# Performance work log

Measured on AMD Instinct MI355X. Metric: run time of the kernel, lower is better.

The kernel has to match this reference:

```python
import jax, jax.numpy as jnp
import numpy as np

B, T, IN, H, OUT = 4096, 256, 2, 50, 2


def _rnn_layer(x, W_ih, W_hh, b_ih, b_hh):
    # x: [B, T, F] -> out: [B, T, H]. Elman RNN: h_t = tanh(W_ih x_t + b_ih + W_hh h_{t-1} + b_hh)
    pre = jnp.einsum('btf,hf->bth', x, W_ih) + b_ih + b_hh  # input projection hoisted out of scan
    h0 = jnp.zeros((x.shape[0], W_hh.shape[0]), dtype=x.dtype)

    def step(h, pre_t):
        h = jnp.tanh(pre_t + h @ W_hh.T)
        return h, h

    _, hs = jax.lax.scan(step, h0, jnp.swapaxes(pre, 0, 1))  # scan over time: [T, B, H]
    return jnp.swapaxes(hs, 0, 1)


def setup_inputs() -> dict:
    key = jax.random.key(0)
    ks = jax.random.split(key, 16)
    s_in = 1.0 / np.sqrt(H)  # torch nn.RNN init: U(-1/sqrt(H), 1/sqrt(H))

    def u(k, shape):
        return jax.random.uniform(k, shape, jnp.float32, -s_in, s_in)

    return {
        'x': jax.random.normal(ks[0], (B, T, IN), jnp.float32),
        'W_ih1': u(ks[1], (H, IN)), 'W_hh1': u(ks[2], (H, H)), 'b_ih1': u(ks[3], (H,)), 'b_hh1': u(ks[4], (H,)),
        'W_ih2': u(ks[5], (H, H)), 'W_hh2': u(ks[6], (H, H)), 'b_ih2': u(ks[7], (H,)), 'b_hh2': u(ks[8], (H,)),
        'W_ih3': u(ks[9], (H, H)), 'W_hh3': u(ks[10], (H, H)), 'b_ih3': u(ks[11], (H,)), 'b_hh3': u(ks[12], (H,)),
        'fc_w': u(ks[13], (OUT, H)), 'fc_b': u(ks[14], (OUT,)),
    }


def reference(x, W_ih1, W_hh1, b_ih1, b_hh1, W_ih2, W_hh2, b_ih2, b_hh2,
              W_ih3, W_hh3, b_ih3, b_hh3, fc_w, fc_b):
    out = _rnn_layer(x, W_ih1, W_hh1, b_ih1, b_hh1)
    out = _rnn_layer(out, W_ih2, W_hh2, b_ih2, b_hh2)
    out = _rnn_layer(out, W_ih3, W_hh3, b_ih3, b_hh3)
    return out[:, -1, :] @ fc_w.T + fc_b  # [B, OUT]
```

## Files before the change

### kernel.cpp

```cpp
#include <hip/hip_runtime.h>
#include <hip/hip_fp16.h>

namespace {

constexpr int T_STEPS = 256;
constexpr int HD = 50;
constexpr int HP = 64;
constexpr int KST = 88;
constexpr int KSTS = 72;
constexpr int BT = 16;
constexpr int NTHR = 768;
constexpr int XST = 34;
constexpr int LAY_SH = BT * KST;
constexpr int SLOT_SH = 3 * LAY_SH;

typedef __attribute__((ext_vector_type(8))) _Float16 f16x8;
typedef __attribute__((ext_vector_type(4))) float f32x4;

__device__ __forceinline__ unsigned short f2h(float x) {
  __half h = __float2half(x);
  return *reinterpret_cast<unsigned short*>(&h);
}
__device__ __forceinline__ float h2f(unsigned short u) {
  __half h;
  *reinterpret_cast<unsigned short*>(&h) = u;
  return __half2float(h);
}
__device__ __forceinline__ float fast_tanh(float x) {
  float e = __expf(2.0f * x);
  return 1.0f - 2.0f * __builtin_amdgcn_rcpf(e + 1.0f);
}

#define MFMA16 __builtin_amdgcn_mfma_f32_16x16x32_f16

__global__ __launch_bounds__(NTHR, 3) void rnn3_kernel(
    const float* __restrict__ x,
    const float* __restrict__ Wih1, const float* __restrict__ Whh1,
    const float* __restrict__ bih1, const float* __restrict__ bhh1,
    const float* __restrict__ Wih2, const float* __restrict__ Whh2,
    const float* __restrict__ bih2, const float* __restrict__ bhh2,
    const float* __restrict__ Wih3, const float* __restrict__ Whh3,
    const float* __restrict__ bih3, const float* __restrict__ bhh3,
    const float* __restrict__ fcw, const float* __restrict__ fcb,
    float* __restrict__ out) {
  __shared__ unsigned short hbuf[3 * SLOT_SH];
  __shared__ float xls[T_STEPS][XST];
  __shared__ unsigned short scr[2][HP * KSTS];

  const int tid = threadIdx.x;
  const int w = tid >> 6;
  const int myL = w >> 2;
  const int wv = w & 3;
  const int lane = tid & 63;
  const int quad = lane >> 4;
  const int l15 = lane & 15;
  const int b0 = blockIdx.x * BT;

  {
    unsigned int* hz = reinterpret_cast<unsigned int*>(hbuf);
    const int n = 3 * SLOT_SH / 2;
    for (int i = tid; i < n; i += NTHR) hz[i] = 0u;
  }
  for (int idx = tid; idx < BT * T_STEPS; idx += NTHR) {
    int b = idx >> 8, t = idx & 255;
    float2 v = *reinterpret_cast<const float2*>(x + (size_t)(b0 + b) * (T_STEPS * 2) + 2 * t);
    xls[t][2 * b] = v.x;
    xls[t][2 * b + 1] = v.y;
  }

  const float* mats[5] = {Whh1, Wih2, Whh2, Wih3, Whh3};
  constexpr int matL[5] = {0, 1, 1, 2, 2};
  constexpr int matS[5] = {0, 0, 1, 0, 1};
  f16x8 wAh[2][2], wAl[2][2];
#pragma unroll
  for (int sl = 0; sl < 2; ++sl)
#pragma unroll
    for (int ks = 0; ks < 2; ++ks) { wAh[sl][ks] = f16x8(0); wAl[sl][ks] = f16x8(0); }

  const int arow = 16 * wv + l15;
#pragma unroll
  for (int m = 0; m < 5; ++m) {
    __syncthreads();
    const float* W = mats[m];
    for (int idx = tid; idx < HP * HP; idx += NTHR) {
      int i = idx >> 6, k = idx & 63;
      float v = (i < HD && k < HD) ? W[i * HD + k] : 0.0f;
      unsigned short hi = f2h(v);
      scr[0][i * KSTS + k] = hi;
      scr[1][i * KSTS + k] = f2h((v - h2f(hi)) * 2048.0f);
    }
    __syncthreads();
    if (myL == matL[m]) {
      const int sl = matS[m];
      const unsigned short* ph = &scr[0][arow * KSTS + 8 * quad];
      const unsigned short* pl = &scr[1][arow * KSTS + 8 * quad];
      wAh[sl][0] = *reinterpret_cast<const f16x8*>(ph);
      wAh[sl][1] = *reinterpret_cast<const f16x8*>(ph + 32);
      wAl[sl][0] = *reinterpret_cast<const f16x8*>(pl);
      wAl[sl][1] = *reinterpret_cast<const f16x8*>(pl + 32);
    }
  }

  const int ic = 16 * wv + 4 * quad;
  const float* bi = (myL == 0) ? bih1 : (myL == 1) ? bih2 : bih3;
  const float* bh = (myL == 0) ? bhh1 : (myL == 1) ? bhh2 : bhh3;
  float wx0[4], wx1[4], bs[4];
#pragma unroll
  for (int r = 0; r < 4; ++r) {
    int i = ic + r;
    bool v = i < HD;
    bs[r] = v ? (bi[i] + bh[i]) : 0.0f;
    wx0[r] = (v && myL == 0) ? Wih1[i * 2 + 0] : 0.0f;
    wx1[r] = (v && myL == 0) ? Wih1[i * 2 + 1] : 0.0f;
  }

  const int selfBuf = myL;
  const int crossBuf = (myL > 0) ? myL - 1 : 0;
  const int ldsOff = l15 * KST + 8 * quad;
  constexpr float INV = 4.8828125e-4f;

  const unsigned short* sbase = hbuf + selfBuf * LAY_SH + ldsOff;
  const unsigned short* cbase = hbuf + crossBuf * LAY_SH + ldsOff;
  unsigned short* wbase = hbuf + myL * LAY_SH + l15 * KST + ic;

  f16x8 pfC0 = f16x8(0), pfC1 = f16x8(0);

  __syncthreads();

  auto step = [&](int s, int wr, int rd, bool act) {
    f16x8 bS0, bS1, pfN0, pfN1;
    if (act) {
      bS0 = *reinterpret_cast<const f16x8*>(sbase + rd * SLOT_SH);
      bS1 = *reinterpret_cast<const f16x8*>(sbase + rd * SLOT_SH + 32);
    }
    if (myL > 0) {
      pfN0 = *reinterpret_cast<const f16x8*>(cbase + rd * SLOT_SH);
      pfN1 = *reinterpret_cast<const f16x8*>(cbase + rd * SLOT_SH + 32);
    }
    if (act) {
      f32x4 c1, c2;
      if (myL == 0) {
        float2 xc = *reinterpret_cast<const float2*>(&xls[s][2 * l15]);
#pragma unroll
        for (int r = 0; r < 4; ++r) {
          c1[r] = bs[r] + wx0[r] * xc.x + wx1[r] * xc.y;
          c2[r] = 0.0f;
        }
        c1 = MFMA16(wAh[0][0], bS0, c1, 0, 0, 0);
        c2 = MFMA16(wAl[0][0], bS0, c2, 0, 0, 0);
        c1 = MFMA16(wAh[0][1], bS1, c1, 0, 0, 0);
        c2 = MFMA16(wAl[0][1], bS1, c2, 0, 0, 0);
      } else {
#pragma unroll
        for (int r = 0; r < 4; ++r) { c1[r] = bs[r]; c2[r] = 0.0f; }
        c1 = MFMA16(wAh[0][0], pfC0, c1, 0, 0, 0);
        c2 = MFMA16(wAl[0][0], pfC0, c2, 0, 0, 0);
        c1 = MFMA16(wAh[0][1], pfC1, c1, 0, 0, 0);
        c2 = MFMA16(wAl[0][1], pfC1, c2, 0, 0, 0);
        c1 = MFMA16(wAh[1][0], bS0, c1, 0, 0, 0);
        c2 = MFMA16(wAl[1][0], bS0, c2, 0, 0, 0);
        c1 = MFMA16(wAh[1][1], bS1, c1, 0, 0, 0);
        c2 = MFMA16(wAl[1][1], bS1, c2, 0, 0, 0);
      }
      unsigned short ht[4];
#pragma unroll
      for (int r = 0; r < 4; ++r) ht[r] = f2h(fast_tanh(c1[r] + c2[r] * INV));
      unsigned int h01 = (unsigned int)ht[0] | ((unsigned int)ht[1] << 16);
      unsigned int h23 = (unsigned int)ht[2] | ((unsigned int)ht[3] << 16);
      *reinterpret_cast<uint2*>(wbase + wr * SLOT_SH) = make_uint2(h01, h23);
    }
    if (myL > 0) { pfC0 = pfN0; pfC1 = pfN1; }
    __syncthreads();
  };

  auto actOf = [&](int s) {
    return (myL == 0) ? (s < T_STEPS)
         : (myL == 1) ? (s >= 2 && s < T_STEPS + 2)
                      : (s >= 4);
  };

  for (int s = 0; s < 4; ++s) step(s, s % 3, (s + 2) % 3, actOf(s));
  int sb = 4;
  for (int it = 0; it < 84; ++it, sb += 3) {
    step(sb + 0, 1, 0, true);
    step(sb + 1, 2, 1, true);
    step(sb + 2, 0, 2, true);
  }
  for (int s = 256; s < 260; ++s) step(s, s % 3, (s + 2) % 3, actOf(s));

  if (tid < BT * 2) {
    int b = tid >> 1, o = tid & 1;
    const unsigned short* h3 = hbuf + 1 * SLOT_SH + 2 * LAY_SH + b * KST;
    float acc = fcb[o];
    for (int i = 0; i < HD; ++i) acc += fcw[o * HD + i] * h2f(h3[i]);
    out[(size_t)(b0 + b) * 2 + o] = acc;
  }
}

}

extern "C" void kernel_launch(void* const* d_in, const int* in_sizes, int n_in,
                              void* d_out, int out_size, void* d_ws, size_t ws_size,
                              hipStream_t stream) {
  const float* x = (const float*)d_in[0];
  const float* Wih1 = (const float*)d_in[1];
  const float* Whh1 = (const float*)d_in[2];
  const float* bih1 = (const float*)d_in[3];
  const float* bhh1 = (const float*)d_in[4];
  const float* Wih2 = (const float*)d_in[5];
  const float* Whh2 = (const float*)d_in[6];
  const float* bih2 = (const float*)d_in[7];
  const float* bhh2 = (const float*)d_in[8];
  const float* Wih3 = (const float*)d_in[9];
  const float* Whh3 = (const float*)d_in[10];
  const float* bih3 = (const float*)d_in[11];
  const float* bhh3 = (const float*)d_in[12];
  const float* fcw = (const float*)d_in[13];
  const float* fcb = (const float*)d_in[14];

  rnn3_kernel<<<4096 / BT, NTHR, 0, stream>>>(x, Wih1, Whh1, bih1, bhh1,
                                              Wih2, Whh2, bih2, bhh2,
                                              Wih3, Whh3, bih3, bhh3,
                                              fcw, fcb, (float*)d_out);
}
```

Measured before the change: 201.7 us.

## Give each RNN layer a single wave computing all four output tiles

The block shrinks from 12 waves (4 per layer, one 16-row tile each) to 3 waves, one per layer. Each wave now keeps all four weight row-tiles in registers and issues four times as many MFMAs per step. The wave reads its own hidden state right after writing it, and the next step's x and cross-layer input are loaded before the barrier. The aim is cheaper per-step barriers with fewer waves and fewer LDS round trips, at the cost of much higher register pressure and less parallelism per block.

```diff
diff --git a/kernel.cpp b/kernel.cpp
--- a/kernel.cpp
+++ b/kernel.cpp
@@ -9,7 +9,7 @@
 constexpr int KST = 88;
 constexpr int KSTS = 72;
 constexpr int BT = 16;
-constexpr int NTHR = 768;
+constexpr int NTHR = 192;
 constexpr int XST = 34;
 constexpr int LAY_SH = BT * KST;
 constexpr int SLOT_SH = 3 * LAY_SH;
@@ -33,7 +33,7 @@
 
 #define MFMA16 __builtin_amdgcn_mfma_f32_16x16x32_f16
 
-__global__ __launch_bounds__(NTHR, 3) void rnn3_kernel(
+__global__ __launch_bounds__(NTHR, 1) void rnn3_kernel(
     const float* __restrict__ x,
     const float* __restrict__ Wih1, const float* __restrict__ Whh1,
     const float* __restrict__ bih1, const float* __restrict__ bhh1,
@@ -48,9 +48,7 @@
   __shared__ unsigned short scr[2][HP * KSTS];
 
   const int tid = threadIdx.x;
-  const int w = tid >> 6;
-  const int myL = w >> 2;
-  const int wv = w & 3;
+  const int myL = tid >> 6;
   const int lane = tid & 63;
   const int quad = lane >> 4;
   const int l15 = lane & 15;
@@ -70,14 +68,15 @@
 
   const float* mats[5] = {Whh1, Wih2, Whh2, Wih3, Whh3};
   constexpr int matL[5] = {0, 1, 1, 2, 2};
-  constexpr int matS[5] = {0, 0, 1, 0, 1};
-  f16x8 wAh[2][2], wAl[2][2];
+  constexpr int matS[5] = {1, 0, 1, 0, 1};
+  f16x8 wAh[2][4][2], wAl[2][4][2];
 #pragma unroll
   for (int sl = 0; sl < 2; ++sl)
 #pragma unroll
-    for (int ks = 0; ks < 2; ++ks) { wAh[sl][ks] = f16x8(0); wAl[sl][ks] = f16x8(0); }
-
-  const int arow = 16 * wv + l15;
+    for (int t = 0; t < 4; ++t)
+#pragma unroll
+      for (int ks = 0; ks < 2; ++ks) { wAh[sl][t][ks] = f16x8(0); wAl[sl][t][ks] = f16x8(0); }
+
 #pragma unroll
   for (int m = 0; m < 5; ++m) {
     __syncthreads();
@@ -92,84 +91,93 @@
     __syncthreads();
     if (myL == matL[m]) {
       const int sl = matS[m];
-      const unsigned short* ph = &scr[0][arow * KSTS + 8 * quad];
-      const unsigned short* pl = &scr[1][arow * KSTS + 8 * quad];
-      wAh[sl][0] = *reinterpret_cast<const f16x8*>(ph);
-      wAh[sl][1] = *reinterpret_cast<const f16x8*>(ph + 32);
-      wAl[sl][0] = *reinterpret_cast<const f16x8*>(pl);
-      wAl[sl][1] = *reinterpret_cast<const f16x8*>(pl + 32);
-    }
-  }
-
-  const int ic = 16 * wv + 4 * quad;
+#pragma unroll
+      for (int t = 0; t < 4; ++t) {
+        const int arow = 16 * t + l15;
+#pragma unroll
+        for (int ks = 0; ks < 2; ++ks) {
+          wAh[sl][t][ks] = *reinterpret_cast<const f16x8*>(&scr[0][arow * KSTS + 32 * ks + 8 * quad]);
+          wAl[sl][t][ks] = *reinterpret_cast<const f16x8*>(&scr[1][arow * KSTS + 32 * ks + 8 * quad]);
+        }
+      }
+    }
+  }
+
   const float* bi = (myL == 0) ? bih1 : (myL == 1) ? bih2 : bih3;
   const float* bh = (myL == 0) ? bhh1 : (myL == 1) ? bhh2 : bhh3;
-  float wx0[4], wx1[4], bs[4];
-#pragma unroll
-  for (int r = 0; r < 4; ++r) {
-    int i = ic + r;
-    bool v = i < HD;
-    bs[r] = v ? (bi[i] + bh[i]) : 0.0f;
-    wx0[r] = (v && myL == 0) ? Wih1[i * 2 + 0] : 0.0f;
-    wx1[r] = (v && myL == 0) ? Wih1[i * 2 + 1] : 0.0f;
-  }
-
-  const int selfBuf = myL;
-  const int crossBuf = (myL > 0) ? myL - 1 : 0;
-  const int ldsOff = l15 * KST + 8 * quad;
+  float bsc[4][4], wx0[4][4], wx1[4][4];
+  f32x4 bsv[4];
+#pragma unroll
+  for (int t = 0; t < 4; ++t)
+#pragma unroll
+    for (int r = 0; r < 4; ++r) {
+      int i = 16 * t + 4 * quad + r;
+      bool v = i < HD;
+      bsc[t][r] = v ? (bi[i] + bh[i]) : 0.0f;
+      wx0[t][r] = (v && myL == 0) ? Wih1[i * 2 + 0] : 0.0f;
+      wx1[t][r] = (v && myL == 0) ? Wih1[i * 2 + 1] : 0.0f;
+      bsv[t][r] = bsc[t][r];
+    }
+
+  const int ldsOffR = l15 * KST + 8 * quad;
+  const unsigned short* sbase = hbuf + myL * LAY_SH + ldsOffR;
+  const unsigned short* cbase = hbuf + ((myL > 0) ? myL - 1 : 0) * LAY_SH + ldsOffR;
+  unsigned short* wbase = hbuf + myL * LAY_SH + l15 * KST + 4 * quad;
   constexpr float INV = 4.8828125e-4f;
 
-  const unsigned short* sbase = hbuf + selfBuf * LAY_SH + ldsOff;
-  const unsigned short* cbase = hbuf + crossBuf * LAY_SH + ldsOff;
-  unsigned short* wbase = hbuf + myL * LAY_SH + l15 * KST + ic;
-
-  f16x8 pfC0 = f16x8(0), pfC1 = f16x8(0);
+  f16x8 bS0 = f16x8(0), bS1 = f16x8(0);
+  f16x8 pf0 = f16x8(0), pf1 = f16x8(0);
+  f32x4 zero4 = {0.f, 0.f, 0.f, 0.f};
 
   __syncthreads();
-
-  auto step = [&](int s, int wr, int rd, bool act) {
-    f16x8 bS0, bS1, pfN0, pfN1;
+  float2 xcur = (myL == 0) ? *reinterpret_cast<const float2*>(&xls[0][2 * l15])
+                           : make_float2(0.f, 0.f);
+
+  auto step = [&](int s, int wr, int rd2, bool act) {
     if (act) {
-      bS0 = *reinterpret_cast<const f16x8*>(sbase + rd * SLOT_SH);
-      bS1 = *reinterpret_cast<const f16x8*>(sbase + rd * SLOT_SH + 32);
-    }
+      f32x4 c1[4], c2[4];
+      if (myL == 0) {
+#pragma unroll
+        for (int t = 0; t < 4; ++t) {
+          f32x4 ci;
+#pragma unroll
+          for (int r = 0; r < 4; ++r) ci[r] = bsc[t][r] + wx0[t][r] * xcur.x + wx1[t][r] * xcur.y;
+          c1[t] = MFMA16(wAh[1][t][0], bS0, ci, 0, 0, 0);
+          c2[t] = MFMA16(wAl[1][t][0], bS0, zero4, 0, 0, 0);
+          c1[t] = MFMA16(wAh[1][t][1], bS1, c1[t], 0, 0, 0);
+          c2[t] = MFMA16(wAl[1][t][1], bS1, c2[t], 0, 0, 0);
+        }
+        int sn = (s + 1 < T_STEPS) ? s + 1 : T_STEPS - 1;
+        xcur = *reinterpret_cast<const float2*>(&xls[sn][2 * l15]);
+      } else {
+#pragma unroll
+        for (int t = 0; t < 4; ++t) {
+          c1[t] = MFMA16(wAh[0][t][0], pf0, bsv[t], 0, 0, 0);
+          c2[t] = MFMA16(wAl[0][t][0], pf0, zero4, 0, 0, 0);
+          c1[t] = MFMA16(wAh[0][t][1], pf1, c1[t], 0, 0, 0);
+          c2[t] = MFMA16(wAl[0][t][1], pf1, c2[t], 0, 0, 0);
+          c1[t] = MFMA16(wAh[1][t][0], bS0, c1[t], 0, 0, 0);
+          c2[t] = MFMA16(wAl[1][t][0], bS0, c2[t], 0, 0, 0);
+          c1[t] = MFMA16(wAh[1][t][1], bS1, c1[t], 0, 0, 0);
+          c2[t] = MFMA16(wAl[1][t][1], bS1, c2[t], 0, 0, 0);
+        }
+      }
+#pragma unroll
+      for (int t = 0; t < 4; ++t) {
+        unsigned short ht[4];
+#pragma unroll
+        for (int r = 0; r < 4; ++r) ht[r] = f2h(fast_tanh(c1[t][r] + c2[t][r] * INV));
+        unsigned int h01 = (unsigned int)ht[0] | ((unsigned int)ht[1] << 16);
+        unsigned int h23 = (unsigned int)ht[2] | ((unsigned int)ht[3] << 16);
+        *reinterpret_cast<uint2*>(wbase + wr * SLOT_SH + 16 * t) = make_uint2(h01, h23);
+      }
+    }
+    bS0 = *reinterpret_cast<const f16x8*>(sbase + wr * SLOT_SH);
+    bS1 = *reinterpret_cast<const f16x8*>(sbase + wr * SLOT_SH + 32);
     if (myL > 0) {
-      pfN0 = *reinterpret_cast<const f16x8*>(cbase + rd * SLOT_SH);
-      pfN1 = *reinterpret_cast<const f16x8*>(cbase + rd * SLOT_SH + 32);
-    }
-    if (act) {
-      f32x4 c1, c2;
-      if (myL == 0) {
-        float2 xc = *reinterpret_cast<const float2*>(&xls[s][2 * l15]);
-#pragma unroll
-        for (int r = 0; r < 4; ++r) {
-          c1[r] = bs[r] + wx0[r] * xc.x + wx1[r] * xc.y;
-          c2[r] = 0.0f;
-        }
-        c1 = MFMA16(wAh[0][0], bS0, c1, 0, 0, 0);
-        c2 = MFMA16(wAl[0][0], bS0, c2, 0, 0, 0);
-        c1 = MFMA16(wAh[0][1], bS1, c1, 0, 0, 0);
-        c2 = MFMA16(wAl[0][1], bS1, c2, 0, 0, 0);
-      } else {
-#pragma unroll
-        for (int r = 0; r < 4; ++r) { c1[r] = bs[r]; c2[r] = 0.0f; }
-        c1 = MFMA16(wAh[0][0], pfC0, c1, 0, 0, 0);
-        c2 = MFMA16(wAl[0][0], pfC0, c2, 0, 0, 0);
-        c1 = MFMA16(wAh[0][1], pfC1, c1, 0, 0, 0);
-        c2 = MFMA16(wAl[0][1], pfC1, c2, 0, 0, 0);
-        c1 = MFMA16(wAh[1][0], bS0, c1, 0, 0, 0);
-        c2 = MFMA16(wAl[1][0], bS0, c2, 0, 0, 0);
-        c1 = MFMA16(wAh[1][1], bS1, c1, 0, 0, 0);
-        c2 = MFMA16(wAl[1][1], bS1, c2, 0, 0, 0);
-      }
-      unsigned short ht[4];
-#pragma unroll
-      for (int r = 0; r < 4; ++r) ht[r] = f2h(fast_tanh(c1[r] + c2[r] * INV));
-      unsigned int h01 = (unsigned int)ht[0] | ((unsigned int)ht[1] << 16);
-      unsigned int h23 = (unsigned int)ht[2] | ((unsigned int)ht[3] << 16);
-      *reinterpret_cast<uint2*>(wbase + wr * SLOT_SH) = make_uint2(h01, h23);
-    }
-    if (myL > 0) { pfC0 = pfN0; pfC1 = pfN1; }
+      pf0 = *reinterpret_cast<const f16x8*>(cbase + rd2 * SLOT_SH);
+      pf1 = *reinterpret_cast<const f16x8*>(cbase + rd2 * SLOT_SH + 32);
+    }
     __syncthreads();
   };
 
@@ -180,8 +188,7 @@
   };
 
   for (int s = 0; s < 4; ++s) step(s, s % 3, (s + 2) % 3, actOf(s));
-  int sb = 4;
-  for (int it = 0; it < 84; ++it, sb += 3) {
+  for (int sb = 4; sb < 256; sb += 3) {
     step(sb + 0, 1, 0, true);
     step(sb + 1, 2, 1, true);
     step(sb + 2, 0, 2, true);
```

Result: slower. 301.4 us (+49.4%).

## Drop split-fp16 weight correction and batch tanh reciprocals per lane

Applied to the files above, without the earlier changes.

Removes the hi/lo fp16 weight split, so each step issues half as many MFMAs and the serial dependency chain per recurrence step gets shorter. The four tanh evaluations per lane now share a single reciprocal through a product trick, with inputs clamped to avoid overflow. The bias is also fed directly as the MFMA accumulator. In exchange, weights are held only in fp16, which lowers accuracy and may push results outside tolerance.

```diff
diff --git a/kernel.cpp b/kernel.cpp
--- a/kernel.cpp
+++ b/kernel.cpp
@@ -25,10 +25,6 @@
   __half h;
   *reinterpret_cast<unsigned short*>(&h) = u;
   return __half2float(h);
-}
-__device__ __forceinline__ float fast_tanh(float x) {
-  float e = __expf(2.0f * x);
-  return 1.0f - 2.0f * __builtin_amdgcn_rcpf(e + 1.0f);
 }
 
 #define MFMA16 __builtin_amdgcn_mfma_f32_16x16x32_f16
@@ -45,7 +41,7 @@
     float* __restrict__ out) {
   __shared__ unsigned short hbuf[3 * SLOT_SH];
   __shared__ float xls[T_STEPS][XST];
-  __shared__ unsigned short scr[2][HP * KSTS];
+  __shared__ unsigned short scr[HP * KSTS];
 
   const int tid = threadIdx.x;
   const int w = tid >> 6;
@@ -71,11 +67,11 @@
   const float* mats[5] = {Whh1, Wih2, Whh2, Wih3, Whh3};
   constexpr int matL[5] = {0, 1, 1, 2, 2};
   constexpr int matS[5] = {0, 0, 1, 0, 1};
-  f16x8 wAh[2][2], wAl[2][2];
+  f16x8 wA[2][2];
 #pragma unroll
   for (int sl = 0; sl < 2; ++sl)
 #pragma unroll
-    for (int ks = 0; ks < 2; ++ks) { wAh[sl][ks] = f16x8(0); wAl[sl][ks] = f16x8(0); }
+    for (int ks = 0; ks < 2; ++ks) wA[sl][ks] = f16x8(0);
 
   const int arow = 16 * wv + l15;
 #pragma unroll
@@ -85,31 +81,27 @@
     for (int idx = tid; idx < HP * HP; idx += NTHR) {
       int i = idx >> 6, k = idx & 63;
       float v = (i < HD && k < HD) ? W[i * HD + k] : 0.0f;
-      unsigned short hi = f2h(v);
-      scr[0][i * KSTS + k] = hi;
-      scr[1][i * KSTS + k] = f2h((v - h2f(hi)) * 2048.0f);
+      scr[i * KSTS + k] = f2h(v);
     }
     __syncthreads();
     if (myL == matL[m]) {
       const int sl = matS[m];
-      const unsigned short* ph = &scr[0][arow * KSTS + 8 * quad];
-      const unsigned short* pl = &scr[1][arow * KSTS + 8 * quad];
-      wAh[sl][0] = *reinterpret_cast<const f16x8*>(ph);
-      wAh[sl][1] = *reinterpret_cast<const f16x8*>(ph + 32);
-      wAl[sl][0] = *reinterpret_cast<const f16x8*>(pl);
-      wAl[sl][1] = *reinterpret_cast<const f16x8*>(pl + 32);
+      const unsigned short* ph = &scr[arow * KSTS + 8 * quad];
+      wA[sl][0] = *reinterpret_cast<const f16x8*>(ph);
+      wA[sl][1] = *reinterpret_cast<const f16x8*>(ph + 32);
     }
   }
 
   const int ic = 16 * wv + 4 * quad;
   const float* bi = (myL == 0) ? bih1 : (myL == 1) ? bih2 : bih3;
   const float* bh = (myL == 0) ? bhh1 : (myL == 1) ? bhh2 : bhh3;
-  float wx0[4], wx1[4], bs[4];
+  float wx0[4], wx1[4];
+  f32x4 bsv;
 #pragma unroll
   for (int r = 0; r < 4; ++r) {
     int i = ic + r;
     bool v = i < HD;
-    bs[r] = v ? (bi[i] + bh[i]) : 0.0f;
+    bsv[r] = v ? (bi[i] + bh[i]) : 0.0f;
     wx0[r] = (v && myL == 0) ? Wih1[i * 2 + 0] : 0.0f;
     wx1[r] = (v && myL == 0) ? Wih1[i * 2 + 1] : 0.0f;
   }
@@ -117,7 +109,6 @@
   const int selfBuf = myL;
   const int crossBuf = (myL > 0) ? myL - 1 : 0;
   const int ldsOff = l15 * KST + 8 * quad;
-  constexpr float INV = 4.8828125e-4f;
 
   const unsigned short* sbase = hbuf + selfBuf * LAY_SH + ldsOff;
   const unsigned short* cbase = hbuf + crossBuf * LAY_SH + ldsOff;
@@ -138,33 +129,33 @@
       pfN1 = *reinterpret_cast<const f16x8*>(cbase + rd * SLOT_SH + 32);
     }
     if (act) {
-      f32x4 c1, c2;
+      f32x4 c;
       if (myL == 0) {
         float2 xc = *reinterpret_cast<const float2*>(&xls[s][2 * l15]);
-#pragma unroll
-        for (int r = 0; r < 4; ++r) {
-          c1[r] = bs[r] + wx0[r] * xc.x + wx1[r] * xc.y;
-          c2[r] = 0.0f;
-        }
-        c1 = MFMA16(wAh[0][0], bS0, c1, 0, 0, 0);
-        c2 = MFMA16(wAl[0][0], bS0, c2, 0, 0, 0);
-        c1 = MFMA16(wAh[0][1], bS1, c1, 0, 0, 0);
-        c2 = MFMA16(wAl[0][1], bS1, c2, 0, 0, 0);
+        f32x4 ci;
+#pragma unroll
+        for (int r = 0; r < 4; ++r) ci[r] = fmaf(wx1[r], xc.y, fmaf(wx0[r], xc.x, bsv[r]));
+        c = MFMA16(wA[0][0], bS0, ci, 0, 0, 0);
+        c = MFMA16(wA[0][1], bS1, c, 0, 0, 0);
       } else {
-#pragma unroll
-        for (int r = 0; r < 4; ++r) { c1[r] = bs[r]; c2[r] = 0.0f; }
-        c1 = MFMA16(wAh[0][0], pfC0, c1, 0, 0, 0);
-        c2 = MFMA16(wAl[0][0], pfC0, c2, 0, 0, 0);
-        c1 = MFMA16(wAh[0][1], pfC1, c1, 0, 0, 0);
-        c2 = MFMA16(wAl[0][1], pfC1, c2, 0, 0, 0);
-        c1 = MFMA16(wAh[1][0], bS0, c1, 0, 0, 0);
-        c2 = MFMA16(wAl[1][0], bS0, c2, 0, 0, 0);
-        c1 = MFMA16(wAh[1][1], bS1, c1, 0, 0, 0);
-        c2 = MFMA16(wAl[1][1], bS1, c2, 0, 0, 0);
+        c = MFMA16(wA[0][0], pfC0, bsv, 0, 0, 0);
+        c = MFMA16(wA[0][1], pfC1, c, 0, 0, 0);
+        c = MFMA16(wA[1][0], bS0, c, 0, 0, 0);
+        c = MFMA16(wA[1][1], bS1, c, 0, 0, 0);
       }
+      float d[4];
+#pragma unroll
+      for (int r = 0; r < 4; ++r) {
+        float xr = __builtin_amdgcn_fmed3f(c[r], -11.0f, 11.0f);
+        d[r] = __expf(2.0f * xr) + 1.0f;
+      }
+      float p01 = d[0] * d[1], p23 = d[2] * d[3];
+      float rp = __builtin_amdgcn_rcpf(p01 * p23);
+      float q01 = rp * p23, q23 = rp * p01;
+      float iv[4] = {q01 * d[1], q01 * d[0], q23 * d[3], q23 * d[2]};
       unsigned short ht[4];
 #pragma unroll
-      for (int r = 0; r < 4; ++r) ht[r] = f2h(fast_tanh(c1[r] + c2[r] * INV));
+      for (int r = 0; r < 4; ++r) ht[r] = f2h(fmaf(-2.0f, iv[r], 1.0f));
       unsigned int h01 = (unsigned int)ht[0] | ((unsigned int)ht[1] << 16);
       unsigned int h23 = (unsigned int)ht[2] | ((unsigned int)ht[3] << 16);
       *reinterpret_cast<uint2*>(wbase + wr * SLOT_SH) = make_uint2(h01, h23);
@@ -180,8 +171,7 @@
   };
 
   for (int s = 0; s < 4; ++s) step(s, s % 3, (s + 2) % 3, actOf(s));
-  int sb = 4;
-  for (int it = 0; it < 84; ++it, sb += 3) {
+  for (int sb = 4; sb < 256; sb += 3) {
     step(sb + 0, 1, 0, true);
     step(sb + 1, 2, 1, true);
     step(sb + 2, 0, 2, true);
```

Result: faster. 196.9 us (-2.4%).
